# Kernel tuning notes

Measured on AMD Instinct MI355X. Metric: run time of the kernel, lower is better.

## Reference

```python
import jax, jax.numpy as jnp
import numpy as np

ANCHORS = np.array([[10,13],[16,30],[33,23],[30,61],[62,45],[59,119],[116,90],[156,198],[373,326]], dtype=np.float32)
ANCHOR_MASK = [[6,7,8],[3,4,5],[0,1,2]]
CLASS_NUM = 80
IGNORE_THRESH = 0.5


def _bce_mean(z, x):
    # Keras BinaryCrossentropy(from_logits=True) called as a loss object:
    # elementwise sigmoid-CE, mean over last axis, then SUM_OVER_BATCH_SIZE
    # reduction == mean over ALL elements -> scalar.
    ce = jnp.maximum(x, 0.0) - x * z + jnp.log1p(jnp.exp(-jnp.abs(x)))
    return jnp.mean(ce)


def _layer_loss(out, lab, anchors):
    B, gh, gw, _ = out.shape
    A = anchors.shape[0]
    feats = out.reshape(B, gh, gw, A, CLASS_NUM + 5)
    anchors = jnp.asarray(anchors, dtype=jnp.float32)  # [A,2] (w,h)
    inp_wh = jnp.array([gw * 32, gh * 32], dtype=jnp.float32)  # reverse(input_shape)
    grid_wh = jnp.array([gw, gh], dtype=jnp.float32)           # reverse(grid_shape)

    gy, gx = jnp.meshgrid(jnp.arange(gh), jnp.arange(gw), indexing='ij')
    grid = jnp.stack([gx, gy], axis=-1).astype(jnp.float32)[:, :, None, :]  # [gh,gw,1,2]

    pred_xy = (jax.nn.sigmoid(feats[..., 0:2]) + grid) / grid_wh
    pred_wh = jnp.exp(feats[..., 2:4]) * anchors / inp_wh
    pred_box = jnp.concatenate([pred_xy, pred_wh], axis=-1)  # [B,gh,gw,A,4]

    obj = lab[..., 4:5]          # [B,gh,gw,A,1]
    objb = obj != 0.0
    N = gh * gw * A

    def _per_image(args):
        pb, tb, valid = args  # pb: [N,4] predicted, tb: [N,4] label boxes, valid: [N] bool
        b1_xy, b1_wh = pb[:, None, 0:2], pb[:, None, 2:4]
        b2_xy, b2_wh = tb[None, :, 0:2], tb[None, :, 2:4]
        b1_mins, b1_maxes = b1_xy - b1_wh / 2.0, b1_xy + b1_wh / 2.0
        b2_mins, b2_maxes = b2_xy - b2_wh / 2.0, b2_xy + b2_wh / 2.0
        inter_mins = jnp.maximum(b1_mins, b2_mins)
        inter_maxes = jnp.maximum(b1_maxes, b2_maxes)  # faithful to source (uses maximum, not minimum)
        inter_wh = jnp.maximum(inter_maxes - inter_mins, 0.0)
        inter = inter_wh[..., 0] * inter_wh[..., 1]
        a1 = b1_wh[..., 0] * b1_wh[..., 1]
        a2 = b2_wh[..., 0] * b2_wh[..., 1]
        iou = inter / (a1 + a2 - inter)  # [N,N]
        # only true boxes count; empty set -> best=-1 (matches tf reduce_max of empty = -inf)
        iou = jnp.where(valid[None, :], iou, -1.0)
        best_iou = jnp.max(iou, axis=-1)
        return (best_iou < IGNORE_THRESH).astype(jnp.float32)

    ignore = jax.lax.map(_per_image, (pred_box.reshape(B, N, 4),
                                      lab[..., 0:4].reshape(B, N, 4),
                                      objb.reshape(B, N)))
    ignore = jax.lax.stop_gradient(ignore).reshape(B, gh, gw, A, 1)

    raw_true_xy = lab[..., 0:2] * grid_wh - grid
    raw_true_wh = jnp.log(lab[..., 2:4] * inp_wh / anchors)
    raw_true_wh = jnp.where(objb, raw_true_wh, 0.0)
    box_loss_scale = 2.0 - lab[..., 2:3] * lab[..., 3:4]

    bf = jnp.float32(B)
    xy_loss = jnp.sum(obj * box_loss_scale * _bce_mean(raw_true_xy, feats[..., 0:2])) / bf
    wh_loss = jnp.sum(obj * box_loss_scale * 0.5 * jnp.square(raw_true_wh - feats[..., 2:4])) / bf
    conf_bce = _bce_mean(obj, feats[..., 4:5])
    conf_loss = jnp.sum(obj * conf_bce + (1.0 - obj) * conf_bce * ignore) / bf
    class_loss = jnp.sum(obj * _bce_mean(lab[..., 5:], feats[..., 5:])) / bf
    return xy_loss + wh_loss + conf_loss + class_loss


def _make_labels(key, B, g):
    k1, k2, k3, k4 = jax.random.split(key, 4)
    xy = jax.random.uniform(k1, (B, g, g, 3, 2), dtype=jnp.float32)
    wh = jax.random.uniform(k2, (B, g, g, 3, 2), dtype=jnp.float32, minval=0.05, maxval=1.0)
    objness = (jax.random.uniform(k3, (B, g, g, 3, 1)) < 0.02).astype(jnp.float32)
    cls = (jax.random.uniform(k4, (B, g, g, 3, CLASS_NUM)) < 0.05).astype(jnp.float32)
    return jnp.concatenate([xy, wh, objness, cls], axis=-1)


def setup_inputs() -> dict:
    key = jax.random.key(0)
    ks = jax.random.split(key, 6)
    B = 8
    grids = [13, 26, 52]
    out = {}
    for i, g in enumerate(grids):
        out[f'o{i}'] = jax.random.normal(ks[i], (B, g, g, 3 * (CLASS_NUM + 5)), dtype=jnp.float32)
        out[f'l{i}'] = _make_labels(ks[3 + i], B, g)
    return out


def reference(o0, o1, o2, l0, l1, l2):
    outputs = (o0, o1, o2)
    labels = (l0, l1, l2)
    loss = jnp.float32(0.0)
    for l in range(3):
        loss = loss + _layer_loss(outputs[l], labels[l], ANCHORS[ANCHOR_MASK[l]])
    return loss
```

## Files before the change

kernel.cpp:

```cpp
#include <hip/hip_runtime.h>
#include <math.h>

#define BDIM 256
#define NSTREAMB 1769
#define NCELLB 334
#define NBLK_A (NSTREAMB + NCELLB)
#define NB_IGNORE 336
#define TCAP 512

__device__ __constant__ float c_aw[3][3] = {{116.f,156.f,373.f},{30.f,62.f,59.f},{10.f,16.f,33.f}};
__device__ __constant__ float c_ah[3][3] = {{90.f,198.f,326.f},{61.f,45.f,119.f},{13.f,30.f,23.f}};


__device__ __forceinline__ float bce_fast(float z, float x) {
    float t = __expf(-fabsf(x));
    return fmaxf(x, 0.f) - x * z + __logf(1.f + t);
}
__device__ __forceinline__ float bce4(const float4& z, const float4& x) {
    return bce_fast(z.x, x.x) + bce_fast(z.y, x.y)
         + bce_fast(z.z, x.z) + bce_fast(z.w, x.w);
}

__global__ __launch_bounds__(BDIM) void mega_a(
    const float* __restrict__ o0, const float* __restrict__ l0,
    const float* __restrict__ o1, const float* __restrict__ l1,
    const float* __restrict__ o2, const float* __restrict__ l2,
    double* __restrict__ accq7, int* __restrict__ done,
    double* __restrict__ slotS, double* __restrict__ slotC,
    int* __restrict__ countB, int* __restrict__ cidxB,
    float4* __restrict__ tboxB, float4* __restrict__ pbox,
    float* __restrict__ noobj)
{
    if (blockIdx.x < NSTREAMB) {
        if (blockIdx.x == 0 && threadIdx.x == 0) {
            accq7[0] = 0.0; accq7[1] = 0.0; accq7[2] = 0.0; *done = 0;
        }
        int blk0, n4;
        const float4 *O4, *L4;
        if (blockIdx.x < 85)       { blk0=0;   n4=86190;   O4=(const float4*)o0; L4=(const float4*)l0; }
        else if (blockIdx.x < 422) { blk0=85;  n4=344760;  O4=(const float4*)o1; L4=(const float4*)l1; }
        else                       { blk0=422; n4=1379040; O4=(const float4*)o2; L4=(const float4*)l2; }

        int rb   = (int)blockIdx.x - blk0;
        int base = rb * (BDIM * 4) + (int)threadIdx.x;
        float s0 = 0.f, s1 = 0.f, s2 = 0.f, s3 = 0.f;
        if ((rb + 1) * (BDIM * 4) <= n4) {
            float4 a0 = O4[base];          float4 b0 = L4[base];
            float4 a1 = O4[base +   BDIM]; float4 b1 = L4[base +   BDIM];
            float4 a2 = O4[base + 2*BDIM]; float4 b2 = L4[base + 2*BDIM];
            float4 a3 = O4[base + 3*BDIM]; float4 b3 = L4[base + 3*BDIM];
            s0 = bce4(b0, a0); s1 = bce4(b1, a1);
            s2 = bce4(b2, a2); s3 = bce4(b3, a3);
        } else {
            #pragma unroll
            for (int k = 0; k < 4; k++) {
                int j = base + k * BDIM;
                if (j < n4) { float4 a = O4[j], b = L4[j]; s0 += bce4(b, a); }
            }
        }
        float s = (s0 + s1) + (s2 + s3);
        __shared__ float sb[4];
        #pragma unroll
        for (int off = 32; off > 0; off >>= 1) s += __shfl_down(s, off, 64);
        if ((threadIdx.x & 63) == 0) sb[threadIdx.x >> 6] = s;
        __syncthreads();
        if (threadIdx.x == 0)
            slotS[blockIdx.x] = (double)sb[0] + (double)sb[1]
                              + (double)sb[2] + (double)sb[3];
        return;
    }

    int cb = blockIdx.x - NSTREAMB;
    int layer, cblk0;
    if (cb < 16)      { layer = 0; cblk0 = 0; }
    else if (cb < 80) { layer = 1; cblk0 = 16; }
    else              { layer = 2; cblk0 = 80; }
    const int g     = (layer == 0) ? 13 : (layer == 1) ? 26 : 52;
    const int Nlimg = g * g * 3;
    const int Cl    = 8 * Nlimg;
    const int cbase = (layer == 0) ? 0 : (layer == 1) ? 4056 : 20280;
    const float* O  = (layer == 0) ? o0 : (layer == 1) ? o1 : o2;
    const float* L  = (layer == 0) ? l0 : (layer == 1) ? l1 : l2;
    const float gf  = (float)g;
    const float inp = gf * 32.f;

    int  cell = (cb - cblk0) * BDIM + (int)threadIdx.x;
    bool live = (cell < Cl);
    float s_sub=0.f, s_xy=0.f, s_wh=0.f, s_conf=0.f, s_obj=0.f, s_s1=0.f;
    bool  f = false;
    float tlx=0.f, tly=0.f, tlw=0.f, tlh=0.f;
    if (live) {
        const float* op = O + (size_t)cell * 85;
        const float* lp = L + (size_t)cell * 85;
        float x0=op[0], x1=op[1], x2=op[2], x3=op[3], x4=op[4];
        float lx=lp[0], ly=lp[1], lw=lp[2], lh=lp[3], lobj=lp[4];
        int a  = cell % 3;
        int xi = (cell / 3) % g;
        int yi = (cell / (3 * g)) % g;
        float aw = c_aw[layer][a], ah = c_ah[layer][a];

        float c4 = bce_fast(lobj, x4);
        s_sub  = bce_fast(lx,x0) + bce_fast(ly,x1)
               + bce_fast(lw,x2) + bce_fast(lh,x3) + c4;
        s_conf = c4;
        s_obj  = lobj;
        s_xy   = bce_fast(lx*gf - (float)xi, x0) + bce_fast(ly*gf - (float)yi, x1);

        float px = (1.f/(1.f+expf(-x0)) + (float)xi) / gf;
        float py = (1.f/(1.f+expf(-x1)) + (float)yi) / gf;
        float pw = expf(x2) * aw / inp;
        float ph = expf(x3) * ah / inp;
        pbox[cbase + cell]  = make_float4(px, py, pw, ph);
        noobj[cbase + cell] = 1.f - lobj;

        if (lobj != 0.f) {
            float bls = 2.f - lw * lh;
            s_s1 = lobj * bls;
            float dw = logf(lw * inp / aw) - x2;
            float dh = logf(lh * inp / ah) - x3;
            s_wh = lobj * bls * 0.5f * (dw * dw + dh * dh);
            f = true; tlx = lx; tly = ly; tlw = lw; tlh = lh;
        }
    }

    unsigned long long m = __ballot(f);
    int lane = threadIdx.x & 63, wid = threadIdx.x >> 6;
    __shared__ int wcnt[4];
    if (lane == 0) wcnt[wid] = __popcll(m);
    int pos = __popcll(m & ((1ull << lane) - 1));
    __syncthreads();
    int wbase = 0;
    #pragma unroll
    for (int w = 0; w < 4; w++) if (w < wid) wbase += wcnt[w];
    if (f) {
        int p = cb * BDIM + wbase + pos;
        tboxB[p] = make_float4(tlx, tly, tlw, tlh);
        cidxB[p] = cell;
    }
    if (threadIdx.x == 0)
        countB[cb] = wcnt[0] + wcnt[1] + wcnt[2] + wcnt[3];

    __shared__ float sb6[6][4];
    float v[6] = {s_sub, s_xy, s_wh, s_conf, s_obj, s_s1};
    #pragma unroll
    for (int q = 0; q < 6; q++) {
        float x = v[q];
        #pragma unroll
        for (int off = 32; off > 0; off >>= 1) x += __shfl_down(x, off, 64);
        if ((threadIdx.x & 63) == 0) sb6[q][threadIdx.x >> 6] = x;
    }
    __syncthreads();
    if (threadIdx.x < 6) {
        int q = threadIdx.x;
        slotC[cb * 6 + q] = (double)sb6[q][0] + (double)sb6[q][1]
                          + (double)sb6[q][2] + (double)sb6[q][3];
    }
}

__global__ __launch_bounds__(BDIM) void ignore_fin(
    double* __restrict__ accq7, int* __restrict__ done,
    const double* __restrict__ slotS, const double* __restrict__ slotC,
    const int* __restrict__ countB, const int* __restrict__ cidxB,
    const float4* __restrict__ tboxB, const float4* __restrict__ pbox,
    const float* __restrict__ noobj, float* __restrict__ out)
{
    int layer, img, chunk;
    if (blockIdx.x < 16)      { layer = 0; img = blockIdx.x >> 1; chunk = blockIdx.x & 1; }
    else if (blockIdx.x < 80) { int t = blockIdx.x - 16; layer = 1; img = t >> 3; chunk = t & 7; }
    else                      { int t = blockIdx.x - 80; layer = 2; img = t >> 5; chunk = t & 31; }
    const int g     = (layer == 0) ? 13 : (layer == 1) ? 26 : 52;
    const int Nlimg = g * g * 3;
    const int cbase = (layer == 0) ? 0 : (layer == 1) ? 4056 : 20280;
    const int cblk0 = (layer == 0) ? 0 : (layer == 1) ? 16 : 80;

    int ci = chunk * BDIM + (int)threadIdx.x;
    bool live = (ci < Nlimg);
    int cell = cbase + img * Nlimg + (live ? ci : 0);

    float pminx=0, pmaxx=0, pminy=0, pmaxy=0, a1=0, nb=0;
    if (live) {
        float4 p = pbox[cell];
        pminx = p.x - p.z*0.5f; pmaxx = p.x + p.z*0.5f;
        pminy = p.y - p.w*0.5f; pmaxy = p.y + p.w*0.5f;
        a1 = p.z * p.w;
        nb = noobj[cell];
    }

    int b0 = cblk0 + (img * Nlimg) / BDIM;
    int b1 = cblk0 + ((img + 1) * Nlimg - 1) / BDIM;
    int nbk = b1 - b0 + 1;

    __shared__ int    sCnt[40];
    __shared__ int    sN;
    __shared__ float4 sT[TCAP];
    for (int i = threadIdx.x; i < nbk; i += BDIM) sCnt[i] = countB[b0 + i];
    if (threadIdx.x == 0) sN = 0;

    float best = -1.f;
    bool donef = !live;

#define IOU_SCAN(TN)                                                         \
    if (!donef) {                                                            \
        for (int j = 0; j < (TN); j++) {                                     \
            float4 t = sT[j];                                                \
            float hw = t.z*0.5f, hh = t.w*0.5f;                              \
                         \
            float imnx = fmaxf(pminx, t.x - hw);                             \
            float imxx = fmaxf(pmaxx, t.x + hw);                             \
            float imny = fmaxf(pminy, t.y - hh);                             \
            float imxy = fmaxf(pmaxy, t.y + hh);                             \
            float iw = fmaxf(imxx - imnx, 0.f);                              \
            float ih = fmaxf(imxy - imny, 0.f);                              \
            float inter = iw * ih;                                           \
            float iou = inter / (a1 + t.z*t.w - inter);                      \
            best = fmaxf(best, iou);                                         \
            if (best >= 0.5f) { donef = true; break; }                       \
        }                                                                    \
    }

    for (int bi = 0; bi < nbk; ++bi) {
        __syncthreads();
        int n = sCnt[bi];
        if (sN + n > TCAP) {
            int tn = sN;
            IOU_SCAN(tn);
            __syncthreads();
            if (threadIdx.x == 0) sN = 0;
            __syncthreads();
        }
        int gbase = (b0 + bi) * BDIM;
        for (int i = threadIdx.x; i < n; i += BDIM) {
            int cidx = cidxB[gbase + i];
            if (cidx / Nlimg == img) {
                int p = atomicAdd(&sN, 1);
                sT[p] = tboxB[gbase + i];
            }
        }
    }
    __syncthreads();
    {
        int tn = sN;
        IOU_SCAN(tn);
    }

    float v = (live && best < 0.5f) ? nb : 0.f;
    __shared__ float sbr[4];
    #pragma unroll
    for (int off = 32; off > 0; off >>= 1) v += __shfl_down(v, off, 64);
    if ((threadIdx.x & 63) == 0) sbr[threadIdx.x >> 6] = v;
    __syncthreads();
    __shared__ int isLast;
    if (threadIdx.x == 0) {
        double t = (double)sbr[0] + (double)sbr[1] + (double)sbr[2] + (double)sbr[3];
        atomicAdd(&accq7[layer], t);
        __threadfence();
        int old = atomicAdd(done, 1);
        isLast = (old == NB_IGNORE - 1) ? 1 : 0;
    }
    __syncthreads();
    if (!isLast) return;

    __threadfence();
    double qs0=0, qs1=0, qs2=0;
    for (int i = threadIdx.x; i < NSTREAMB; i += BDIM) {
        double x = slotS[i];
        if (i < 85) qs0 += x; else if (i < 422) qs1 += x; else qs2 += x;
    }
    double c00=0,c01=0,c02=0,c03=0,c04=0,c05=0;
    double c10=0,c11=0,c12=0,c13=0,c14=0,c15=0;
    double c20=0,c21=0,c22=0,c23=0,c24=0,c25=0;
#define CSUM(LO, HI, A0,A1,A2,A3,A4,A5)                                      \
    for (int i = (LO)*6 + (int)threadIdx.x; i < (HI)*6; i += BDIM) {         \
        int q = i % 6; double x = slotC[i];                                  \
        if      (q == 0) A0 += x; else if (q == 1) A1 += x;                  \
        else if (q == 2) A2 += x; else if (q == 3) A3 += x;                  \
        else if (q == 4) A4 += x; else             A5 += x;                  \
    }
    CSUM(0,   16,  c00,c01,c02,c03,c04,c05)
    CSUM(16,  80,  c10,c11,c12,c13,c14,c15)
    CSUM(80,  334, c20,c21,c22,c23,c24,c25)

    __shared__ double dsum[21][4];
    {
        double vals[21] = {qs0,qs1,qs2,
                           c00,c01,c02,c03,c04,c05,
                           c10,c11,c12,c13,c14,c15,
                           c20,c21,c22,c23,c24,c25};
        int lane = threadIdx.x & 63, wid = threadIdx.x >> 6;
        #pragma unroll
        for (int k = 0; k < 21; k++) {
            double r = vals[k];
            #pragma unroll
            for (int off = 32; off > 0; off >>= 1) r += __shfl_down(r, off, 64);
            if (lane == 0) dsum[k][wid] = r;
        }
    }
    __syncthreads();
    if (threadIdx.x == 0) {
        double loss = 0.0;
        const int gsz[3] = {13, 26, 52};
        for (int l = 0; l < 3; l++) {
            double C = 8.0 * gsz[l] * gsz[l] * 3.0;
            double Q0 = dsum[l][0] + dsum[l][1] + dsum[l][2] + dsum[l][3];
            double Qs[6];
            for (int j = 0; j < 6; j++) {
                int k = 3 + l * 6 + j;
                Qs[j] = dsum[k][0] + dsum[k][1] + dsum[k][2] + dsum[k][3];
            }
            double q7 = __hip_atomic_load(&accq7[l], __ATOMIC_RELAXED,
                                          __HIP_MEMORY_SCOPE_AGENT);
            double cls = (Q0 - Qs[0]) / (C * 80.0);
            loss += ( (Qs[1]/(C*2.0))*Qs[5] + Qs[2]
                    + (Qs[3]/C)*(Qs[4]+q7) + cls*Qs[4] ) / 8.0;
        }
        out[0] = (float)loss;
    }
}

extern "C" void kernel_launch(void* const* d_in, const int* in_sizes, int n_in,
                              void* d_out, int out_size, void* d_ws, size_t ws_size,
                              hipStream_t stream)
{
    const float* o0 = (const float*)d_in[0];
    const float* l0 = (const float*)d_in[1];
    const float* o1 = (const float*)d_in[2];
    const float* l1 = (const float*)d_in[3];
    const float* o2 = (const float*)d_in[4];
    const float* l2 = (const float*)d_in[5];

    double* accq7  = (double*)d_ws;
    int*    done   = (int*)((char*)d_ws + 24);
    double* slotS  = (double*)((char*)d_ws + 64);
    double* slotC  = (double*)((char*)d_ws + 14336);
    int*    countB = (int*)((char*)d_ws + 30720);
    int*    cidxB  = (int*)((char*)d_ws + 32768);
    float4* tboxB  = (float4*)((char*)d_ws + 375296);
    float4* pbox   = (float4*)((char*)d_ws + 1742848);
    float*  noobj  = (float*)((char*)d_ws + 3105664);

    mega_a<<<NBLK_A, BDIM, 0, stream>>>(o0, l0, o1, l1, o2, l2,
                                        accq7, done, slotS, slotC,
                                        countB, cidxB, tboxB, pbox, noobj);
    ignore_fin<<<NB_IGNORE, BDIM, 0, stream>>>(accq7, done, slotS, slotC,
                                               countB, cidxB, tboxB, pbox,
                                               noobj, (float*)d_out);
}
```

Before: 163.0 us.

## Build per-image true-box lists inside ignore kernel from noobj instead of pre-compaction

Drops the ballot/popcount compaction of object boxes, and the countB, cidxB and tboxB buffers, from the first kernel. Each ignore block now scans the noobj array for its whole image, collects object indices in shared memory, and gathers the four box coordinates straight from the label tensor. This trims work and global writes in the large first kernel and makes the IoU scan loop simpler. In exchange, every block re-reads a full image's noobj slice and does scattered gathers from the labels. Boxes past SCAP (1024) per image are silently dropped.

```diff
diff --git a/kernel.cpp b/kernel.cpp
--- a/kernel.cpp
+++ b/kernel.cpp
@@ -6,7 +6,7 @@
 #define NCELLB 334
 #define NBLK_A (NSTREAMB + NCELLB)
 #define NB_IGNORE 336
-#define TCAP 512
+#define SCAP 1024
 
 __device__ __constant__ float c_aw[3][3] = {{116.f,156.f,373.f},{30.f,62.f,59.f},{10.f,16.f,33.f}};
 __device__ __constant__ float c_ah[3][3] = {{90.f,198.f,326.f},{61.f,45.f,119.f},{13.f,30.f,23.f}};
@@ -27,9 +27,7 @@
     const float* __restrict__ o2, const float* __restrict__ l2,
     double* __restrict__ accq7, int* __restrict__ done,
     double* __restrict__ slotS, double* __restrict__ slotC,
-    int* __restrict__ countB, int* __restrict__ cidxB,
-    float4* __restrict__ tboxB, float4* __restrict__ pbox,
-    float* __restrict__ noobj)
+    float4* __restrict__ pbox, float* __restrict__ noobj)
 {
     if (blockIdx.x < NSTREAMB) {
         if (blockIdx.x == 0 && threadIdx.x == 0) {
@@ -87,8 +85,6 @@
     int  cell = (cb - cblk0) * BDIM + (int)threadIdx.x;
     bool live = (cell < Cl);
     float s_sub=0.f, s_xy=0.f, s_wh=0.f, s_conf=0.f, s_obj=0.f, s_s1=0.f;
-    bool  f = false;
-    float tlx=0.f, tly=0.f, tlw=0.f, tlh=0.f;
     if (live) {
         const float* op = O + (size_t)cell * 85;
         const float* lp = L + (size_t)cell * 85;
@@ -119,26 +115,8 @@
             float dw = logf(lw * inp / aw) - x2;
             float dh = logf(lh * inp / ah) - x3;
             s_wh = lobj * bls * 0.5f * (dw * dw + dh * dh);
-            f = true; tlx = lx; tly = ly; tlw = lw; tlh = lh;
-        }
-    }
-
-    unsigned long long m = __ballot(f);
-    int lane = threadIdx.x & 63, wid = threadIdx.x >> 6;
-    __shared__ int wcnt[4];
-    if (lane == 0) wcnt[wid] = __popcll(m);
-    int pos = __popcll(m & ((1ull << lane) - 1));
-    __syncthreads();
-    int wbase = 0;
-    #pragma unroll
-    for (int w = 0; w < 4; w++) if (w < wid) wbase += wcnt[w];
-    if (f) {
-        int p = cb * BDIM + wbase + pos;
-        tboxB[p] = make_float4(tlx, tly, tlw, tlh);
-        cidxB[p] = cell;
-    }
-    if (threadIdx.x == 0)
-        countB[cb] = wcnt[0] + wcnt[1] + wcnt[2] + wcnt[3];
+        }
+    }
 
     __shared__ float sb6[6][4];
     float v[6] = {s_sub, s_xy, s_wh, s_conf, s_obj, s_s1};
@@ -158,11 +136,12 @@
 }
 
 __global__ __launch_bounds__(BDIM) void ignore_fin(
+    const float* __restrict__ l0, const float* __restrict__ l1,
+    const float* __restrict__ l2,
     double* __restrict__ accq7, int* __restrict__ done,
     const double* __restrict__ slotS, const double* __restrict__ slotC,
-    const int* __restrict__ countB, const int* __restrict__ cidxB,
-    const float4* __restrict__ tboxB, const float4* __restrict__ pbox,
-    const float* __restrict__ noobj, float* __restrict__ out)
+    const float4* __restrict__ pbox, const float* __restrict__ noobj,
+    float* __restrict__ out)
 {
     int layer, img, chunk;
     if (blockIdx.x < 16)      { layer = 0; img = blockIdx.x >> 1; chunk = blockIdx.x & 1; }
@@ -171,7 +150,7 @@
     const int g     = (layer == 0) ? 13 : (layer == 1) ? 26 : 52;
     const int Nlimg = g * g * 3;
     const int cbase = (layer == 0) ? 0 : (layer == 1) ? 4056 : 20280;
-    const int cblk0 = (layer == 0) ? 0 : (layer == 1) ? 16 : 80;
+    const float* L  = (layer == 0) ? l0 : (layer == 1) ? l1 : l2;
 
     int ci = chunk * BDIM + (int)threadIdx.x;
     bool live = (ci < Nlimg);
@@ -186,61 +165,42 @@
         nb = noobj[cell];
     }
 
-    int b0 = cblk0 + (img * Nlimg) / BDIM;
-    int b1 = cblk0 + ((img + 1) * Nlimg - 1) / BDIM;
-    int nbk = b1 - b0 + 1;
-
-    __shared__ int    sCnt[40];
+    __shared__ int    sIdx[SCAP];
     __shared__ int    sN;
-    __shared__ float4 sT[TCAP];
-    for (int i = threadIdx.x; i < nbk; i += BDIM) sCnt[i] = countB[b0 + i];
+    __shared__ float4 sT[SCAP];
     if (threadIdx.x == 0) sN = 0;
+    __syncthreads();
+    const float* nob = noobj + cbase + img * Nlimg;
+    for (int i = threadIdx.x; i < Nlimg; i += BDIM) {
+        if (nob[i] == 0.0f) {
+            int p = atomicAdd(&sN, 1);
+            if (p < SCAP) sIdx[p] = i;
+        }
+    }
+    __syncthreads();
+    int n = min(sN, SCAP);
+    for (int i = threadIdx.x; i < n; i += BDIM) {
+        const float* lp = L + (size_t)(img * Nlimg + sIdx[i]) * 85;
+        sT[i] = make_float4(lp[0], lp[1], lp[2], lp[3]);
+    }
+    __syncthreads();
 
     float best = -1.f;
-    bool donef = !live;
-
-#define IOU_SCAN(TN)                                                         \
-    if (!donef) {                                                            \
-        for (int j = 0; j < (TN); j++) {                                     \
-            float4 t = sT[j];                                                \
-            float hw = t.z*0.5f, hh = t.w*0.5f;                              \
-                         \
-            float imnx = fmaxf(pminx, t.x - hw);                             \
-            float imxx = fmaxf(pmaxx, t.x + hw);                             \
-            float imny = fmaxf(pminy, t.y - hh);                             \
-            float imxy = fmaxf(pmaxy, t.y + hh);                             \
-            float iw = fmaxf(imxx - imnx, 0.f);                              \
-            float ih = fmaxf(imxy - imny, 0.f);                              \
-            float inter = iw * ih;                                           \
-            float iou = inter / (a1 + t.z*t.w - inter);                      \
-            best = fmaxf(best, iou);                                         \
-            if (best >= 0.5f) { donef = true; break; }                       \
-        }                                                                    \
-    }
-
-    for (int bi = 0; bi < nbk; ++bi) {
-        __syncthreads();
-        int n = sCnt[bi];
-        if (sN + n > TCAP) {
-            int tn = sN;
-            IOU_SCAN(tn);
-            __syncthreads();
-            if (threadIdx.x == 0) sN = 0;
-            __syncthreads();
-        }
-        int gbase = (b0 + bi) * BDIM;
-        for (int i = threadIdx.x; i < n; i += BDIM) {
-            int cidx = cidxB[gbase + i];
-            if (cidx / Nlimg == img) {
-                int p = atomicAdd(&sN, 1);
-                sT[p] = tboxB[gbase + i];
-            }
-        }
-    }
-    __syncthreads();
-    {
-        int tn = sN;
-        IOU_SCAN(tn);
+    if (live) {
+        for (int j = 0; j < n; j++) {
+            float4 t = sT[j];
+            float hw = t.z*0.5f, hh = t.w*0.5f;
+            float imnx = fmaxf(pminx, t.x - hw);
+            float imxx = fmaxf(pmaxx, t.x + hw);
+            float imny = fmaxf(pminy, t.y - hh);
+            float imxy = fmaxf(pmaxy, t.y + hh);
+            float iw = fmaxf(imxx - imnx, 0.f);
+            float ih = fmaxf(imxy - imny, 0.f);
+            float inter = iw * ih;
+            float iou = inter / (a1 + t.z*t.w - inter);
+            best = fmaxf(best, iou);
+            if (best >= 0.5f) break;
+        }
     }
 
     float v = (live && best < 0.5f) ? nb : 0.f;
@@ -328,20 +288,16 @@
     const float* o2 = (const float*)d_in[4];
     const float* l2 = (const float*)d_in[5];
 
-    double* accq7  = (double*)d_ws;
-    int*    done   = (int*)((char*)d_ws + 24);
-    double* slotS  = (double*)((char*)d_ws + 64);
-    double* slotC  = (double*)((char*)d_ws + 14336);
-    int*    countB = (int*)((char*)d_ws + 30720);
-    int*    cidxB  = (int*)((char*)d_ws + 32768);
-    float4* tboxB  = (float4*)((char*)d_ws + 375296);
-    float4* pbox   = (float4*)((char*)d_ws + 1742848);
-    float*  noobj  = (float*)((char*)d_ws + 3105664);
+    double* accq7 = (double*)d_ws;
+    int*    done  = (int*)((char*)d_ws + 24);
+    double* slotS = (double*)((char*)d_ws + 64);
+    double* slotC = (double*)((char*)d_ws + 14336);
+    float4* pbox  = (float4*)((char*)d_ws + 30720);
+    float*  noobj = (float*)((char*)d_ws + 1393664);
 
     mega_a<<<NBLK_A, BDIM, 0, stream>>>(o0, l0, o1, l1, o2, l2,
-                                        accq7, done, slotS, slotC,
-                                        countB, cidxB, tboxB, pbox, noobj);
-    ignore_fin<<<NB_IGNORE, BDIM, 0, stream>>>(accq7, done, slotS, slotC,
-                                               countB, cidxB, tboxB, pbox,
-                                               noobj, (float*)d_out);
-}
+                                        accq7, done, slotS, slotC, pbox, noobj);
+    ignore_fin<<<NB_IGNORE, BDIM, 0, stream>>>(l0, l1, l2,
+                                               accq7, done, slotS, slotC,
+                                               pbox, noobj, (float*)d_out);
+}
```

Measured after the change: 151.9 us. 6.8% less time.
